# Optimization experiments

Measured on AMD Instinct MI355X. Metric: run time of the kernel, lower is better.

## Reference

```python
import jax, jax.numpy as jnp
import numpy as np

DIM = 512
HEADS = 8
DK = DIM // HEADS
MAX_LEN = 22118
EPS = 1e-5


def _layernorm(h, g, b):
    m = jnp.mean(h, axis=-1, keepdims=True)
    v = jnp.mean((h - m) ** 2, axis=-1, keepdims=True)
    return (h - m) / jnp.sqrt(v + EPS) * g + b


def setup_inputs() -> dict:
    key = jax.random.key(0)
    ks = jax.random.split(key, 16)
    B, S = 4, 2048
    xavier = lambda k, shp: jax.random.normal(k, shp, jnp.float32) * np.sqrt(2.0 / (shp[0] + shp[1]))
    return {
        "x": jax.random.normal(ks[0], (B, S, DIM), jnp.float32),
        "vis_data": jax.random.normal(ks[1], (B, S, DIM), jnp.float32),
        "coord1": jax.random.randint(ks[2], (B, S), 0, MAX_LEN, jnp.int32),
        "coord2": jax.random.randint(ks[3], (B, S), 0, MAX_LEN, jnp.int32),
        "emb1": jax.random.normal(ks[4], (MAX_LEN, DIM // 2), jnp.float32) * 0.02,
        "emb2": jax.random.normal(ks[5], (MAX_LEN, DIM // 2), jnp.float32) * 0.02,
        "wq": xavier(ks[6], (DIM, DIM)), "bq": jnp.zeros((DIM,), jnp.float32),
        "wk": xavier(ks[7], (DIM, DIM)), "bk": jnp.zeros((DIM,), jnp.float32),
        "wv": xavier(ks[8], (DIM, DIM)), "bv": jnp.zeros((DIM,), jnp.float32),
        "w1": xavier(ks[9], (DIM, DIM)), "b1": jnp.zeros((DIM,), jnp.float32),
        "g1": jnp.ones((DIM,), jnp.float32), "beta1": jnp.zeros((DIM,), jnp.float32),
        "w2": xavier(ks[10], (DIM, DIM)), "b2": jnp.zeros((DIM,), jnp.float32),
        "g2": jnp.ones((DIM,), jnp.float32), "beta2": jnp.zeros((DIM,), jnp.float32),
    }


def reference(x, vis_data, coord1, coord2, emb1, emb2, wq, bq, wk, bk, wv, bv,
              w1, b1, g1, beta1, w2, b2, g2, beta2):
    B, S, _ = x.shape
    # learned positional encoding: concat of two coordinate embeddings
    pos = jnp.concatenate([emb1[coord1], emb2[coord2]], axis=-1)  # [B,S,DIM]
    xp = x + pos
    # Q/K from vis_data, V from position-encoded x
    q = (vis_data @ wq + bq).reshape(B, S, HEADS, DK)
    k = (vis_data @ wk + bk).reshape(B, S, HEADS, DK)
    v = (xp @ wv + bv).reshape(B, S, HEADS, DK)
    scores = jnp.einsum("bqhd,bkhd->bhqk", q, k) / np.sqrt(DK).astype(np.float32)
    attn = jax.nn.softmax(scores, axis=-1)  # dropout is identity in eval
    out = jnp.einsum("bhqk,bkhd->bqhd", attn, v).reshape(B, S, DIM)
    # post-attention MLP stack (self.layer)
    h = jax.nn.leaky_relu(out @ w1 + b1, negative_slope=0.2)
    h = _layernorm(h, g1, beta1)
    h = jax.nn.leaky_relu(h @ w2 + b2, negative_slope=0.2)
    h = _layernorm(h, g2, beta2)
    return h
```

## Files before the change

kernel.cpp:

```cpp
#include <hip/hip_runtime.h>

#define DIM 512
#define SEQ 2048
#define MROWS 8192

typedef short short8 __attribute__((ext_vector_type(8)));
typedef float floatx4 __attribute__((ext_vector_type(4)));

__device__ __forceinline__ ushort f2bf(float f) {
  union { float f; unsigned u; } v; v.f = f;
  unsigned r = v.u + 0x7fff + ((v.u >> 16) & 1);
  return (ushort)(r >> 16);
}
__device__ __forceinline__ float bf2f(ushort u) {
  union { unsigned u; float f; } v; v.u = ((unsigned)u) << 16;
  return v.f;
}

__global__ __launch_bounds__(256) void prep_wtrans_kernel(
    const float* __restrict__ x, const float* __restrict__ vis,
    const int* __restrict__ c1, const int* __restrict__ c2,
    const float* __restrict__ e1, const float* __restrict__ e2,
    const float* __restrict__ wq, const float* __restrict__ wk,
    const float* __restrict__ wv, const float* __restrict__ w1,
    const float* __restrict__ w2,
    ushort* __restrict__ xp_bf, ushort* __restrict__ vis_bf,
    ushort* __restrict__ wt_qkv, ushort* __restrict__ wt1,
    ushort* __restrict__ wt2) {
  __shared__ float Ls[64 * 65];
  if (blockIdx.x < 4096) {
    int gid = blockIdx.x * 256 + threadIdx.x;
    int row = gid >> 7;
    int col = (gid & 127) * 4;
    float4 vv = *(const float4*)(vis + (size_t)row * 512 + col);
    ushort4 vb; vb.x = f2bf(vv.x); vb.y = f2bf(vv.y); vb.z = f2bf(vv.z); vb.w = f2bf(vv.w);
    *(ushort4*)(vis_bf + (size_t)row * 512 + col) = vb;
    float4 p;
    if (col < 256) p = *(const float4*)(e1 + (size_t)c1[row] * 256 + col);
    else           p = *(const float4*)(e2 + (size_t)c2[row] * 256 + col - 256);
    float4 xv = *(const float4*)(x + (size_t)row * 512 + col);
    ushort4 xb; xb.x = f2bf(xv.x + p.x); xb.y = f2bf(xv.y + p.y);
    xb.z = f2bf(xv.z + p.z); xb.w = f2bf(xv.w + p.w);
    *(ushort4*)(xp_bf + (size_t)row * 512 + col) = xb;
  } else {
    int bid = blockIdx.x - 4096;
    int mid = bid >> 6;
    int tile = bid & 63;
    int k0 = (tile >> 3) * 64, n0 = (tile & 7) * 64;
    const float* W = mid == 0 ? wq : mid == 1 ? wk : mid == 2 ? wv : mid == 3 ? w1 : w2;
    ushort* outp = mid < 3 ? (wt_qkv + (size_t)mid * 512 * 512) : (mid == 3 ? wt1 : wt2);
    float scale = (mid == 0) ? 0.125f : 1.0f;
    int r = threadIdx.x >> 4, c4 = (threadIdx.x & 15) * 4;
#pragma unroll
    for (int i = 0; i < 4; i++) {
      int row = i * 16 + r;
      float4 wv4 = *(const float4*)(W + (size_t)(k0 + row) * 512 + n0 + c4);
      Ls[row * 65 + c4 + 0] = wv4.x * scale;
      Ls[row * 65 + c4 + 1] = wv4.y * scale;
      Ls[row * 65 + c4 + 2] = wv4.z * scale;
      Ls[row * 65 + c4 + 3] = wv4.w * scale;
    }
    __syncthreads();
    int n = threadIdx.x >> 2, kc = (threadIdx.x & 3) * 16;
    ushort pk[16];
#pragma unroll
    for (int i = 0; i < 16; i++) pk[i] = f2bf(Ls[(kc + i) * 65 + n]);
    ushort* op = outp + (size_t)(n0 + n) * 512 + k0 + kc;
    *(uint4*)op = *(uint4*)pk;
    *(uint4*)(op + 8) = *(uint4*)(pk + 8);
  }
}

template <bool LEAKY>
__global__ __launch_bounds__(256, 4) void gemm_mfma(
    const ushort* __restrict__ A01, const ushort* __restrict__ A2,
    const ushort* __restrict__ Wt,
    const float* __restrict__ bias0, const float* __restrict__ bias1,
    const float* __restrict__ bias2,
    ushort* __restrict__ out0, ushort* __restrict__ out1,
    ushort* __restrict__ out2, float s0scale) {
  __shared__ __align__(16) ushort Sm[12288];
  ushort* As = Sm;
  ushort* Bs = Sm + 4096;
  int t = threadIdx.x;
  int seg = blockIdx.x >> 2;
  int nloc0 = (blockIdx.x & 3) * 128;
  int n0w = blockIdx.x * 128;
  int m0 = blockIdx.y * 64;
  const ushort* A = (seg < 2) ? A01 : A2;
  const float* bias = seg == 0 ? bias0 : seg == 1 ? bias1 : bias2;
  ushort* out = seg == 0 ? out0 : seg == 1 ? out1 : out2;
  float bscale = seg == 0 ? s0scale : 1.0f;

  int w = t >> 6, lane = t & 63;
  int wm = (w & 1) * 32, wn = (w >> 1) * 64;
  int quad = lane >> 4, lcol = lane & 15;
  int arow = t >> 2, ach = (t & 3) * 2;
  int brow = t >> 1, bch = (t & 1) * 4;

  floatx4 acc[2][4] = {};

  for (int k0 = 0; k0 < 512; k0 += 64) {
    __syncthreads();
#pragma unroll
    for (int i = 0; i < 2; i++) {
      int ch = ach + i;
      *(uint4*)(&As[arow * 64 + (ch ^ (arow & 7)) * 8]) =
          *(const uint4*)(A + (size_t)(m0 + arow) * 512 + k0 + ch * 8);
    }
#pragma unroll
    for (int j = 0; j < 4; j++) {
      int ch = bch + j;
      *(uint4*)(&Bs[brow * 64 + (ch ^ (brow & 7)) * 8]) =
          *(const uint4*)(Wt + (size_t)(n0w + brow) * 512 + k0 + ch * 8);
    }
    __syncthreads();
#pragma unroll
    for (int kc = 0; kc < 2; kc++) {
      int pch = ((kc * 4 + quad) ^ (lcol & 7)) * 8;
      short8 af[2], bfr[4];
#pragma unroll
      for (int i = 0; i < 2; i++)
        af[i] = *(const short8*)(&As[(wm + i * 16 + lcol) * 64 + pch]);
#pragma unroll
      for (int i = 0; i < 4; i++)
        bfr[i] = *(const short8*)(&Bs[(wn + i * 16 + lcol) * 64 + pch]);
#pragma unroll
      for (int mt = 0; mt < 2; mt++)
#pragma unroll
        for (int nt = 0; nt < 4; nt++)
          acc[mt][nt] = __builtin_amdgcn_mfma_f32_16x16x32_bf16(
              af[mt], bfr[nt], acc[mt][nt], 0, 0, 0);
    }
  }

  __syncthreads();
  float* Ls = (float*)Sm + w * 1088;
  int rr = lane >> 2, cc = (lane & 3) * 16;
#pragma unroll
  for (int mt = 0; mt < 2; mt++) {
#pragma unroll
    for (int nt = 0; nt < 4; nt++) {
      float bv = bias[nloc0 + wn + nt * 16 + lcol] * bscale;
#pragma unroll
      for (int r = 0; r < 4; r++) {
        float vv = acc[mt][nt][r] + bv;
        if (LEAKY) vv = vv >= 0.f ? vv : 0.2f * vv;
        Ls[(quad * 4 + r) * 68 + nt * 16 + lcol] = vv;
      }
    }
    asm volatile("s_waitcnt lgkmcnt(0)" ::: "memory");
    ushort pk[16];
#pragma unroll
    for (int i = 0; i < 16; i += 4) {
      float4 fv = *(const float4*)(&Ls[rr * 68 + cc + i]);
      pk[i] = f2bf(fv.x); pk[i + 1] = f2bf(fv.y);
      pk[i + 2] = f2bf(fv.z); pk[i + 3] = f2bf(fv.w);
    }
    ushort* op = out + (size_t)(m0 + wm + mt * 16 + rr) * 512 + nloc0 + wn + cc;
    *(uint4*)op = *(uint4*)pk;
    *(uint4*)(op + 8) = *(uint4*)(pk + 8);
    asm volatile("s_waitcnt lgkmcnt(0)" ::: "memory");
  }
}

__global__ __launch_bounds__(256, 2) void attn_mfma_kernel(
    const ushort* __restrict__ q, const ushort* __restrict__ k,
    const ushort* __restrict__ v, ushort* __restrict__ out) {
  __shared__ __align__(16) ushort Ks[128 * 64];
  __shared__ __align__(16) ushort Vt[64 * 128];
  __shared__ __align__(16) ushort Ps[4 * 32 * 64];
  int t = threadIdx.x;
  int blk = blockIdx.x;
  int qt = blk & 15, h = (blk >> 4) & 7, b = blk >> 7;
  int wave = t >> 6, lane = t & 63, quad = lane >> 4, lcol = lane & 15;
  int q0 = qt * 128 + wave * 32;
  const size_t base = (size_t)b * SEQ * 512 + h * 64;

  short8 qf[2][2];
#pragma unroll
  for (int qm = 0; qm < 2; qm++)
#pragma unroll
    for (int kc = 0; kc < 2; kc++)
      qf[qm][kc] = *(const short8*)(
          q + base + (size_t)(q0 + qm * 16 + lcol) * 512 + kc * 32 + quad * 8);

  floatx4 O[2][4] = {};
  float lsum[2][4] = {};

  ushort* Pw = Ps + wave * (32 * 64);
  int krow = t >> 1, khalf = t & 1;
  int pl = t & 63, dg = t >> 6;

  for (int kt = 0; kt < SEQ; kt += 128) {
    __syncthreads();
#pragma unroll
    for (int j = 0; j < 4; j++) {
      int ch = khalf * 4 + j;
      *(uint4*)(&Ks[krow * 64 + (ch ^ (krow & 7)) * 8]) =
          *(const uint4*)(k + base + (size_t)(kt + krow) * 512 + ch * 8);
    }
    {
      uint4 va[2], vb[2];
      const ushort* vr0 = v + base + (size_t)(kt + 2 * pl) * 512 + dg * 16;
      const ushort* vr1 = vr0 + 512;
      va[0] = *(const uint4*)(vr0); va[1] = *(const uint4*)(vr0 + 8);
      vb[0] = *(const uint4*)(vr1); vb[1] = *(const uint4*)(vr1 + 8);
      const ushort* a0 = (const ushort*)va;
      const ushort* a1 = (const ushort*)vb;
#pragma unroll
      for (int i = 0; i < 16; i++) {
        int dim = dg * 16 + i;
        unsigned pack = (unsigned)a0[i] | ((unsigned)a1[i] << 16);
        int pch = (pl >> 2) ^ (dim & 7);
        *(unsigned*)(&Vt[dim * 128 + pch * 8 + (pl & 3) * 2]) = pack;
      }
    }
    __syncthreads();

#pragma unroll
    for (int half = 0; half < 2; half++) {
#pragma unroll
      for (int qm = 0; qm < 2; qm++) {
        floatx4 S[4] = {};
#pragma unroll
        for (int kc = 0; kc < 2; kc++) {
          int pch = ((kc * 4 + quad) ^ (lcol & 7)) * 8;
#pragma unroll
          for (int jt4 = 0; jt4 < 4; jt4++) {
            int jrow = (half * 4 + jt4) * 16 + lcol;
            short8 kf = *(const short8*)(&Ks[jrow * 64 + pch]);
            S[jt4] = __builtin_amdgcn_mfma_f32_16x16x32_bf16(
                qf[qm][kc], kf, S[jt4], 0, 0, 0);
          }
        }
#pragma unroll
        for (int jt4 = 0; jt4 < 4; jt4++)
#pragma unroll
          for (int r = 0; r < 4; r++) {
            float p = __expf(S[jt4][r]);
            lsum[qm][r] += p;
            int prow = qm * 16 + quad * 4 + r;
            int pcol = jt4 * 16 + lcol;
            int pch2 = (pcol >> 3) ^ (prow & 7);
            Pw[prow * 64 + pch2 * 8 + (pcol & 7)] =
                (ushort)(__float_as_uint(p) >> 16);
          }
      }
      asm volatile("s_waitcnt lgkmcnt(0)" ::: "memory");
#pragma unroll
      for (int qm = 0; qm < 2; qm++) {
#pragma unroll
        for (int kc = 0; kc < 2; kc++) {
          short8 pf = *(const short8*)(
              &Pw[(qm * 16 + lcol) * 64 + ((kc * 4 + quad) ^ (lcol & 7)) * 8]);
#pragma unroll
          for (int nt = 0; nt < 4; nt++) {
            int dim = nt * 16 + lcol;
            int ch = half * 8 + kc * 4 + quad;
            short8 vf = *(const short8*)(&Vt[dim * 128 + (ch ^ (lcol & 7)) * 8]);
            O[qm][nt] = __builtin_amdgcn_mfma_f32_16x16x32_bf16(
                pf, vf, O[qm][nt], 0, 0, 0);
          }
        }
      }
    }
  }

#pragma unroll
  for (int qm = 0; qm < 2; qm++)
#pragma unroll
    for (int r = 0; r < 4; r++) {
#pragma unroll
      for (int m = 1; m <= 8; m <<= 1)
        lsum[qm][r] += __shfl_xor(lsum[qm][r], m, 64);
      lsum[qm][r] = 1.f / lsum[qm][r];
    }
#pragma unroll
  for (int qm = 0; qm < 2; qm++)
#pragma unroll
    for (int nt = 0; nt < 4; nt++)
#pragma unroll
      for (int r = 0; r < 4; r++)
        out[base + (size_t)(q0 + qm * 16 + quad * 4 + r) * 512 + nt * 16 + lcol] =
            f2bf(O[qm][nt][r] * lsum[qm][r]);
}

template <bool OUTF32>
__global__ __launch_bounds__(256) void ln_kernel(
    const ushort* __restrict__ h, const float* __restrict__ g,
    const float* __restrict__ beta, void* __restrict__ outv) {
  int wave = threadIdx.x >> 6, lane = threadIdx.x & 63;
  int row = blockIdx.x * 4 + wave;
  uint4 raw = *(const uint4*)(h + (size_t)row * 512 + lane * 8);
  const ushort* hu = (const ushort*)&raw;
  float vals[8];
#pragma unroll
  for (int i = 0; i < 8; i++) vals[i] = bf2f(hu[i]);
  float sum = 0.f;
#pragma unroll
  for (int i = 0; i < 8; i++) sum += vals[i];
#pragma unroll
  for (int off = 32; off >= 1; off >>= 1) sum += __shfl_xor(sum, off, 64);
  float mean = sum * (1.f / 512.f);
  float vs = 0.f;
#pragma unroll
  for (int i = 0; i < 8; i++) { float d = vals[i] - mean; vs += d * d; }
#pragma unroll
  for (int off = 32; off >= 1; off >>= 1) vs += __shfl_xor(vs, off, 64);
  float rstd = rsqrtf(vs * (1.f / 512.f) + 1e-5f);
  float4 gv0 = *(const float4*)(g + lane * 8);
  float4 gv1 = *(const float4*)(g + lane * 8 + 4);
  float4 bv0 = *(const float4*)(beta + lane * 8);
  float4 bv1 = *(const float4*)(beta + lane * 8 + 4);
  float gr[8] = {gv0.x, gv0.y, gv0.z, gv0.w, gv1.x, gv1.y, gv1.z, gv1.w};
  float br[8] = {bv0.x, bv0.y, bv0.z, bv0.w, bv1.x, bv1.y, bv1.z, bv1.w};
  float res[8];
#pragma unroll
  for (int i = 0; i < 8; i++) res[i] = (vals[i] - mean) * rstd * gr[i] + br[i];
  if (OUTF32) {
    float* op = (float*)outv + (size_t)row * 512 + lane * 8;
    float4 o0, o1;
    o0.x = res[0]; o0.y = res[1]; o0.z = res[2]; o0.w = res[3];
    o1.x = res[4]; o1.y = res[5]; o1.z = res[6]; o1.w = res[7];
    *(float4*)op = o0; *(float4*)(op + 4) = o1;
  } else {
    ushort* op = (ushort*)outv + (size_t)row * 512 + lane * 8;
    ushort4 o0, o1;
    o0.x = f2bf(res[0]); o0.y = f2bf(res[1]); o0.z = f2bf(res[2]); o0.w = f2bf(res[3]);
    o1.x = f2bf(res[4]); o1.y = f2bf(res[5]); o1.z = f2bf(res[6]); o1.w = f2bf(res[7]);
    *(ushort4*)op = o0; *(ushort4*)(op + 4) = o1;
  }
}

extern "C" void kernel_launch(void* const* d_in, const int* in_sizes, int n_in,
                              void* d_out, int out_size, void* d_ws,
                              size_t ws_size, hipStream_t stream) {
  (void)in_sizes; (void)n_in; (void)out_size; (void)ws_size;
  const float* x     = (const float*)d_in[0];
  const float* vis   = (const float*)d_in[1];
  const int*   c1    = (const int*)d_in[2];
  const int*   c2    = (const int*)d_in[3];
  const float* e1    = (const float*)d_in[4];
  const float* e2    = (const float*)d_in[5];
  const float* wq    = (const float*)d_in[6];
  const float* bq    = (const float*)d_in[7];
  const float* wk    = (const float*)d_in[8];
  const float* bk    = (const float*)d_in[9];
  const float* wv    = (const float*)d_in[10];
  const float* bv    = (const float*)d_in[11];
  const float* w1    = (const float*)d_in[12];
  const float* b1    = (const float*)d_in[13];
  const float* g1    = (const float*)d_in[14];
  const float* beta1 = (const float*)d_in[15];
  const float* w2    = (const float*)d_in[16];
  const float* b2    = (const float*)d_in[17];
  const float* g2    = (const float*)d_in[18];
  const float* beta2 = (const float*)d_in[19];
  float* out = (float*)d_out;
  ushort* ws = (ushort*)d_ws;

  const size_t BUF = (size_t)MROWS * 512;
  ushort* xp_bf  = ws;
  ushort* vis_bf = ws + BUF;
  ushort* q_bf   = ws + 2 * BUF;
  ushort* k_bf   = ws + 3 * BUF;
  ushort* v_bf   = ws + 4 * BUF;
  ushort* wt_qkv = ws + 5 * BUF;
  ushort* wt1    = wt_qkv + 1536 * 512;
  ushort* wt2    = wt1 + 512 * 512;
  ushort* attn_bf = vis_bf;
  ushort* h1_bf   = xp_bf;
  ushort* ln1_bf  = q_bf;
  ushort* h2_bf   = k_bf;

  prep_wtrans_kernel<<<4416, 256, 0, stream>>>(
      x, vis, c1, c2, e1, e2, wq, wk, wv, w1, w2, xp_bf, vis_bf, wt_qkv, wt1, wt2);
  gemm_mfma<false><<<dim3(12, 128), 256, 0, stream>>>(
      vis_bf, xp_bf, wt_qkv, bq, bk, bv, q_bf, k_bf, v_bf, 0.125f);
  attn_mfma_kernel<<<512, 256, 0, stream>>>(q_bf, k_bf, v_bf, attn_bf);
  gemm_mfma<true><<<dim3(4, 128), 256, 0, stream>>>(
      attn_bf, attn_bf, wt1, b1, b1, b1, h1_bf, h1_bf, h1_bf, 1.0f);
  ln_kernel<false><<<2048, 256, 0, stream>>>(h1_bf, g1, beta1, ln1_bf);
  gemm_mfma<true><<<dim3(4, 128), 256, 0, stream>>>(
      ln1_bf, ln1_bf, wt2, b2, b2, b2, h2_bf, h2_bf, h2_bf, 1.0f);
  ln_kernel<true><<<2048, 256, 0, stream>>>(h2_bf, g2, beta2, out);
}
```

Baseline: 272.0 us.

## Load GEMM operands directly from global memory and emit head-major QKV for attention

The GEMM no longer stages A/B tiles through LDS with barriers. Each wave loads its MFMA fragments straight from global memory, relying on cache hits for reuse, and the occupancy hint drops from 4 to 3. The QKV projection now writes Q/K/V in a head-major [B,H,S,64] layout, so attention reads contiguous K/V tiles. The attention inner loops are reordered so each K/V fragment read from LDS feeds two MFMAs, one per query sub-tile. The risk is that direct global loads make redundant memory traffic and lose the LDS reuse the old version had.

```diff
diff --git a/kernel.cpp b/kernel.cpp
--- a/kernel.cpp
+++ b/kernel.cpp
@@ -71,17 +71,15 @@
   }
 }
 
-template <bool LEAKY>
-__global__ __launch_bounds__(256, 4) void gemm_mfma(
+template <bool LEAKY, bool HEADMAJOR>
+__global__ __launch_bounds__(256, 3) void gemm_direct(
     const ushort* __restrict__ A01, const ushort* __restrict__ A2,
     const ushort* __restrict__ Wt,
     const float* __restrict__ bias0, const float* __restrict__ bias1,
     const float* __restrict__ bias2,
     ushort* __restrict__ out0, ushort* __restrict__ out1,
     ushort* __restrict__ out2, float s0scale) {
-  __shared__ __align__(16) ushort Sm[12288];
-  ushort* As = Sm;
-  ushort* Bs = Sm + 4096;
+  __shared__ __align__(16) float Ls[4 * 1088];
   int t = threadIdx.x;
   int seg = blockIdx.x >> 2;
   int nloc0 = (blockIdx.x & 3) * 128;
@@ -95,47 +93,35 @@
   int w = t >> 6, lane = t & 63;
   int wm = (w & 1) * 32, wn = (w >> 1) * 64;
   int quad = lane >> 4, lcol = lane & 15;
-  int arow = t >> 2, ach = (t & 3) * 2;
-  int brow = t >> 1, bch = (t & 1) * 4;
+
+  const ushort* Ar0 = A + (size_t)(m0 + wm + lcol) * 512 + quad * 8;
+  const ushort* Ar1 = Ar0 + 16 * 512;
+  const ushort* Br0 = Wt + (size_t)(n0w + wn + lcol) * 512 + quad * 8;
+  const ushort* Br1 = Br0 + 16 * 512;
+  const ushort* Br2 = Br0 + 32 * 512;
+  const ushort* Br3 = Br0 + 48 * 512;
 
   floatx4 acc[2][4] = {};
 
-  for (int k0 = 0; k0 < 512; k0 += 64) {
-    __syncthreads();
-#pragma unroll
-    for (int i = 0; i < 2; i++) {
-      int ch = ach + i;
-      *(uint4*)(&As[arow * 64 + (ch ^ (arow & 7)) * 8]) =
-          *(const uint4*)(A + (size_t)(m0 + arow) * 512 + k0 + ch * 8);
-    }
-#pragma unroll
-    for (int j = 0; j < 4; j++) {
-      int ch = bch + j;
-      *(uint4*)(&Bs[brow * 64 + (ch ^ (brow & 7)) * 8]) =
-          *(const uint4*)(Wt + (size_t)(n0w + brow) * 512 + k0 + ch * 8);
-    }
-    __syncthreads();
-#pragma unroll
-    for (int kc = 0; kc < 2; kc++) {
-      int pch = ((kc * 4 + quad) ^ (lcol & 7)) * 8;
-      short8 af[2], bfr[4];
-#pragma unroll
-      for (int i = 0; i < 2; i++)
-        af[i] = *(const short8*)(&As[(wm + i * 16 + lcol) * 64 + pch]);
-#pragma unroll
-      for (int i = 0; i < 4; i++)
-        bfr[i] = *(const short8*)(&Bs[(wn + i * 16 + lcol) * 64 + pch]);
-#pragma unroll
-      for (int mt = 0; mt < 2; mt++)
-#pragma unroll
-        for (int nt = 0; nt < 4; nt++)
-          acc[mt][nt] = __builtin_amdgcn_mfma_f32_16x16x32_bf16(
-              af[mt], bfr[nt], acc[mt][nt], 0, 0, 0);
-    }
-  }
-
-  __syncthreads();
-  float* Ls = (float*)Sm + w * 1088;
+#pragma unroll 4
+  for (int k = 0; k < 512; k += 32) {
+    short8 a0 = *(const short8*)(Ar0 + k);
+    short8 a1 = *(const short8*)(Ar1 + k);
+    short8 b0 = *(const short8*)(Br0 + k);
+    short8 b1 = *(const short8*)(Br1 + k);
+    short8 b2 = *(const short8*)(Br2 + k);
+    short8 b3 = *(const short8*)(Br3 + k);
+    acc[0][0] = __builtin_amdgcn_mfma_f32_16x16x32_bf16(a0, b0, acc[0][0], 0, 0, 0);
+    acc[0][1] = __builtin_amdgcn_mfma_f32_16x16x32_bf16(a0, b1, acc[0][1], 0, 0, 0);
+    acc[0][2] = __builtin_amdgcn_mfma_f32_16x16x32_bf16(a0, b2, acc[0][2], 0, 0, 0);
+    acc[0][3] = __builtin_amdgcn_mfma_f32_16x16x32_bf16(a0, b3, acc[0][3], 0, 0, 0);
+    acc[1][0] = __builtin_amdgcn_mfma_f32_16x16x32_bf16(a1, b0, acc[1][0], 0, 0, 0);
+    acc[1][1] = __builtin_amdgcn_mfma_f32_16x16x32_bf16(a1, b1, acc[1][1], 0, 0, 0);
+    acc[1][2] = __builtin_amdgcn_mfma_f32_16x16x32_bf16(a1, b2, acc[1][2], 0, 0, 0);
+    acc[1][3] = __builtin_amdgcn_mfma_f32_16x16x32_bf16(a1, b3, acc[1][3], 0, 0, 0);
+  }
+
+  float* Lw = Ls + w * 1088;
   int rr = lane >> 2, cc = (lane & 3) * 16;
 #pragma unroll
   for (int mt = 0; mt < 2; mt++) {
@@ -146,18 +132,27 @@
       for (int r = 0; r < 4; r++) {
         float vv = acc[mt][nt][r] + bv;
         if (LEAKY) vv = vv >= 0.f ? vv : 0.2f * vv;
-        Ls[(quad * 4 + r) * 68 + nt * 16 + lcol] = vv;
+        Lw[(quad * 4 + r) * 68 + nt * 16 + lcol] = vv;
       }
     }
     asm volatile("s_waitcnt lgkmcnt(0)" ::: "memory");
     ushort pk[16];
 #pragma unroll
     for (int i = 0; i < 16; i += 4) {
-      float4 fv = *(const float4*)(&Ls[rr * 68 + cc + i]);
+      float4 fv = *(const float4*)(&Lw[rr * 68 + cc + i]);
       pk[i] = f2bf(fv.x); pk[i + 1] = f2bf(fv.y);
       pk[i + 2] = f2bf(fv.z); pk[i + 3] = f2bf(fv.w);
     }
-    ushort* op = out + (size_t)(m0 + wm + mt * 16 + rr) * 512 + nloc0 + wn + cc;
+    ushort* op;
+    int m = m0 + wm + mt * 16 + rr;
+    if (HEADMAJOR) {
+      int nseg = nloc0 + wn + cc;
+      int h = nseg >> 6, d = nseg & 63;
+      int b = m >> 11, s = m & 2047;
+      op = out + (((size_t)b * 8 + h) * 2048 + s) * 64 + d;
+    } else {
+      op = out + (size_t)m * 512 + nloc0 + wn + cc;
+    }
     *(uint4*)op = *(uint4*)pk;
     *(uint4*)(op + 8) = *(uint4*)(pk + 8);
     asm volatile("s_waitcnt lgkmcnt(0)" ::: "memory");
@@ -175,7 +170,8 @@
   int qt = blk & 15, h = (blk >> 4) & 7, b = blk >> 7;
   int wave = t >> 6, lane = t & 63, quad = lane >> 4, lcol = lane & 15;
   int q0 = qt * 128 + wave * 32;
-  const size_t base = (size_t)b * SEQ * 512 + h * 64;
+  const size_t hbase = ((size_t)b * 8 + h) * (SEQ * 64);
+  const size_t obase = (size_t)b * SEQ * 512 + h * 64;
 
   short8 qf[2][2];
 #pragma unroll
@@ -183,29 +179,31 @@
 #pragma unroll
     for (int kc = 0; kc < 2; kc++)
       qf[qm][kc] = *(const short8*)(
-          q + base + (size_t)(q0 + qm * 16 + lcol) * 512 + kc * 32 + quad * 8);
+          q + hbase + (size_t)(q0 + qm * 16 + lcol) * 64 + kc * 32 + quad * 8);
 
   floatx4 O[2][4] = {};
   float lsum[2][4] = {};
 
   ushort* Pw = Ps + wave * (32 * 64);
-  int krow = t >> 1, khalf = t & 1;
   int pl = t & 63, dg = t >> 6;
 
   for (int kt = 0; kt < SEQ; kt += 128) {
     __syncthreads();
-#pragma unroll
-    for (int j = 0; j < 4; j++) {
-      int ch = khalf * 4 + j;
-      *(uint4*)(&Ks[krow * 64 + (ch ^ (krow & 7)) * 8]) =
-          *(const uint4*)(k + base + (size_t)(kt + krow) * 512 + ch * 8);
-    }
     {
+      const ushort* kbase = k + hbase + (size_t)kt * 64;
+#pragma unroll
+      for (int i = 0; i < 4; i++) {
+        int id = i * 256 + t;
+        int krow = id >> 3, ch = id & 7;
+        *(uint4*)(&Ks[krow * 64 + (ch ^ (krow & 7)) * 8]) =
+            *(const uint4*)(kbase + id * 8);
+      }
+    }
+    {
+      const ushort* vr0 = v + hbase + (size_t)(kt + 2 * pl) * 64 + dg * 16;
       uint4 va[2], vb[2];
-      const ushort* vr0 = v + base + (size_t)(kt + 2 * pl) * 512 + dg * 16;
-      const ushort* vr1 = vr0 + 512;
       va[0] = *(const uint4*)(vr0); va[1] = *(const uint4*)(vr0 + 8);
-      vb[0] = *(const uint4*)(vr1); vb[1] = *(const uint4*)(vr1 + 8);
+      vb[0] = *(const uint4*)(vr0 + 64); vb[1] = *(const uint4*)(vr0 + 72);
       const ushort* a0 = (const ushort*)va;
       const ushort* a1 = (const ushort*)vb;
 #pragma unroll
@@ -220,25 +218,27 @@
 
 #pragma unroll
     for (int half = 0; half < 2; half++) {
-#pragma unroll
-      for (int qm = 0; qm < 2; qm++) {
-        floatx4 S[4] = {};
-#pragma unroll
-        for (int kc = 0; kc < 2; kc++) {
-          int pch = ((kc * 4 + quad) ^ (lcol & 7)) * 8;
-#pragma unroll
-          for (int jt4 = 0; jt4 < 4; jt4++) {
-            int jrow = (half * 4 + jt4) * 16 + lcol;
-            short8 kf = *(const short8*)(&Ks[jrow * 64 + pch]);
-            S[jt4] = __builtin_amdgcn_mfma_f32_16x16x32_bf16(
-                qf[qm][kc], kf, S[jt4], 0, 0, 0);
-          }
+      floatx4 S[2][4] = {};
+#pragma unroll
+      for (int kc = 0; kc < 2; kc++) {
+        int pch = ((kc * 4 + quad) ^ (lcol & 7)) * 8;
+#pragma unroll
+        for (int jt4 = 0; jt4 < 4; jt4++) {
+          int jrow = (half * 4 + jt4) * 16 + lcol;
+          short8 kf = *(const short8*)(&Ks[jrow * 64 + pch]);
+          S[0][jt4] = __builtin_amdgcn_mfma_f32_16x16x32_bf16(
+              qf[0][kc], kf, S[0][jt4], 0, 0, 0);
+          S[1][jt4] = __builtin_amdgcn_mfma_f32_16x16x32_bf16(
+              qf[1][kc], kf, S[1][jt4], 0, 0, 0);
         }
+      }
+#pragma unroll
+      for (int qm = 0; qm < 2; qm++)
 #pragma unroll
         for (int jt4 = 0; jt4 < 4; jt4++)
 #pragma unroll
           for (int r = 0; r < 4; r++) {
-            float p = __expf(S[jt4][r]);
+            float p = __expf(S[qm][jt4][r]);
             lsum[qm][r] += p;
             int prow = qm * 16 + quad * 4 + r;
             int pcol = jt4 * 16 + lcol;
@@ -246,22 +246,21 @@
             Pw[prow * 64 + pch2 * 8 + (pcol & 7)] =
                 (ushort)(__float_as_uint(p) >> 16);
           }
-      }
       asm volatile("s_waitcnt lgkmcnt(0)" ::: "memory");
 #pragma unroll
-      for (int qm = 0; qm < 2; qm++) {
-#pragma unroll
-        for (int kc = 0; kc < 2; kc++) {
-          short8 pf = *(const short8*)(
-              &Pw[(qm * 16 + lcol) * 64 + ((kc * 4 + quad) ^ (lcol & 7)) * 8]);
-#pragma unroll
-          for (int nt = 0; nt < 4; nt++) {
-            int dim = nt * 16 + lcol;
-            int ch = half * 8 + kc * 4 + quad;
-            short8 vf = *(const short8*)(&Vt[dim * 128 + (ch ^ (lcol & 7)) * 8]);
-            O[qm][nt] = __builtin_amdgcn_mfma_f32_16x16x32_bf16(
-                pf, vf, O[qm][nt], 0, 0, 0);
-          }
+      for (int kc = 0; kc < 2; kc++) {
+        int ppch = ((kc * 4 + quad) ^ (lcol & 7)) * 8;
+        short8 pf0 = *(const short8*)(&Pw[(0 * 16 + lcol) * 64 + ppch]);
+        short8 pf1 = *(const short8*)(&Pw[(1 * 16 + lcol) * 64 + ppch]);
+        int ch = half * 8 + kc * 4 + quad;
+        int vch = (ch ^ (lcol & 7)) * 8;
+#pragma unroll
+        for (int nt = 0; nt < 4; nt++) {
+          short8 vf = *(const short8*)(&Vt[(nt * 16 + lcol) * 128 + vch]);
+          O[0][nt] = __builtin_amdgcn_mfma_f32_16x16x32_bf16(
+              pf0, vf, O[0][nt], 0, 0, 0);
+          O[1][nt] = __builtin_amdgcn_mfma_f32_16x16x32_bf16(
+              pf1, vf, O[1][nt], 0, 0, 0);
         }
       }
     }
@@ -282,7 +281,7 @@
     for (int nt = 0; nt < 4; nt++)
 #pragma unroll
       for (int r = 0; r < 4; r++)
-        out[base + (size_t)(q0 + qm * 16 + quad * 4 + r) * 512 + nt * 16 + lcol] =
+        out[obase + (size_t)(q0 + qm * 16 + quad * 4 + r) * 512 + nt * 16 + lcol] =
             f2bf(O[qm][nt][r] * lsum[qm][r]);
 }
 
@@ -376,13 +375,13 @@
 
   prep_wtrans_kernel<<<4416, 256, 0, stream>>>(
       x, vis, c1, c2, e1, e2, wq, wk, wv, w1, w2, xp_bf, vis_bf, wt_qkv, wt1, wt2);
-  gemm_mfma<false><<<dim3(12, 128), 256, 0, stream>>>(
+  gemm_direct<false, true><<<dim3(12, 128), 256, 0, stream>>>(
       vis_bf, xp_bf, wt_qkv, bq, bk, bv, q_bf, k_bf, v_bf, 0.125f);
   attn_mfma_kernel<<<512, 256, 0, stream>>>(q_bf, k_bf, v_bf, attn_bf);
-  gemm_mfma<true><<<dim3(4, 128), 256, 0, stream>>>(
+  gemm_direct<true, false><<<dim3(4, 128), 256, 0, stream>>>(
       attn_bf, attn_bf, wt1, b1, b1, b1, h1_bf, h1_bf, h1_bf, 1.0f);
   ln_kernel<false><<<2048, 256, 0, stream>>>(h1_bf, g1, beta1, ln1_bf);
-  gemm_mfma<true><<<dim3(4, 128), 256, 0, stream>>>(
+  gemm_direct<true, false><<<dim3(4, 128), 256, 0, stream>>>(
       ln1_bf, ln1_bf, wt2, b2, b2, b2, h2_bf, h2_bf, h2_bf, 1.0f);
   ln_kernel<true><<<2048, 256, 0, stream>>>(h2_bf, g2, beta2, out);
 }
```

Result: slower. 333.3 us (+22.6%).
